# Kernel optimization log

Hardware: AMD Instinct MI355X
Metric: run time of the kernel (lower is better)

Reference implementation:

```python
import jax, jax.numpy as jnp
import numpy as np

# Module constants (from init_kwargs)
MAP_BBOX = (-5.0, -5.0, 5.0, 5.0)  # h1, w1, h2, w2
V_BBOX = (0.0, 3.0)
MAP_RES = (64, 64)
V_RES = 8
XYZ_TO_H, XYZ_TO_W, XYZ_TO_V = 0, 1, 2
SCALE = 4
PCN_H = 64


def mish(x):
    return x * jnp.tanh(jax.nn.softplus(x))


def conv_d2(x, w):
    # 3x3 conv, dilation 2, padding 2, stride 1, no bias (NCHW / OIHW)
    return jax.lax.conv_general_dilated(
        x, w, window_strides=(1, 1), padding=((2, 2), (2, 2)),
        rhs_dilation=(2, 2), dimension_numbers=('NCHW', 'OIHW', 'NCHW'))


def maxpool3s2(x):
    # MaxPool2d(kernel=3, stride=2, padding=1); torch pads with -inf
    return jax.lax.reduce_window(
        x, -jnp.inf, jax.lax.max,
        window_dimensions=(1, 1, 3, 3), window_strides=(1, 1, 2, 2),
        padding=((0, 0), (0, 0), (1, 1), (1, 1)))


def setup_inputs() -> dict:
    key = jax.random.key(0)
    k1, k2, k3, k4, k5 = jax.random.split(key, 5)
    N, H, W = 64, 256, 256
    B = 8
    return {
        'rgb': jax.random.normal(k1, (N, 3, H, W), dtype=jnp.float32),
        'surf_xyz': jax.random.normal(k2, (N, 3, H, W), dtype=jnp.float32),
        'W1': jax.random.normal(k3, (PCN_H, 3, 3, 3), dtype=jnp.float32) * 0.1,
        'W2': jax.random.normal(k4, (PCN_H, PCN_H, 3, 3), dtype=jnp.float32) * 0.05,
        'index': jax.random.randint(k5, (N,), 0, B, dtype=jnp.int32),
        'batch_size': B,
    }


def reference(rgb, surf_xyz, W1, W2, index, batch_size):
    N, _, H, W = surf_xyz.shape
    s = SCALE
    Hs, Ws = H // s, W // s

    # avg_pool2d(rgb, 4)
    surf_rgb = rgb.reshape(N, 3, Hs, s, Ws, s).mean(axis=(3, 5))
    # subsampled xyz: surf_xyz[:, :, 2::4, 2::4]
    sxyz = surf_xyz[:, :, s // 2::s, s // 2::s]  # (N,3,Hs,Ws)
    _index = jnp.broadcast_to(index[:, None, None], (N, Hs, Ws))

    # rgb_conv_net: conv -> mish -> maxpool -> conv -> mish -> maxpool (dropout=0)
    feat = maxpool3s2(mish(conv_d2(rgb, W1)))
    feat = maxpool3s2(mish(conv_d2(feat, W2)))  # (N, h, Hs, Ws)

    # flatten  (valid_points is None path)
    hdim = feat.shape[1]
    flat_features = feat.transpose(0, 2, 3, 1).reshape(-1, hdim)   # (M, h)
    flat_xyz = sxyz.transpose(0, 2, 3, 1).reshape(-1, 3)           # (M, 3)
    flat_rgb = surf_rgb.transpose(0, 2, 3, 1).reshape(-1, 3)       # (M, 3)
    flat_index = _index.reshape(-1)                                # (M,)

    # coord_to_grid (float->int cast truncates toward zero, matching torch .long())
    map_h, map_w = MAP_RES
    h1, w1, h2, w2 = MAP_BBOX
    v1, v2 = V_BBOX
    hs = ((flat_xyz[:, XYZ_TO_H] - h1) * map_h / (h2 - h1)).astype(jnp.int32)
    ws = ((flat_xyz[:, XYZ_TO_W] - w1) * map_w / (w2 - w1)).astype(jnp.int32)
    vs = ((flat_xyz[:, XYZ_TO_V] - v1) * V_RES / (v2 - v1)).astype(jnp.int32)
    valid = ((hs >= 0) & (hs < map_h) & (ws >= 0) & (ws < map_w)
             & (vs >= 0) & (vs < V_RES))

    B, V = batch_size, V_RES
    P = B * V * map_h * map_w
    lin = ((flat_index * V + vs) * map_h + hs) * map_w + ws
    # route invalid points to a dummy segment that gets dropped
    lin_safe = jnp.where(valid, lin, P)

    sums = jax.ops.segment_sum(flat_features, lin_safe, num_segments=P + 1)[:P]
    rgbs = jax.ops.segment_sum(flat_rgb, lin_safe, num_segments=P + 1)[:P]
    counts = jax.ops.segment_sum(
        jnp.ones_like(lin_safe), lin_safe, num_segments=P + 1)[:P]

    feature_map = sums.reshape(B, V, map_h, map_w, hdim).transpose(0, 4, 1, 2, 3)
    rgb_map = rgbs.reshape(B, V, map_h, map_w, 3).transpose(0, 4, 1, 2, 3)
    feature_counts = counts.reshape(B, V, map_h, map_w)[:, None]
    return feature_map, feature_counts, rgb_map
```

## Files before the change

kernel.cpp:

```cpp
#include <hip/hip_runtime.h>
#include <hip/hip_bf16.h>
#include <math.h>

#define N_IMG 64
#define CH    64
#define F1_R  136
#define F1_C  136
#define F1_IMG_STRIDE ((size_t)F1_R * F1_C * 64)
#define F1_ROW_STRIDE (F1_C * 64)
#define FEAT1_BYTES ((size_t)N_IMG * F1_IMG_STRIDE * 2)
#define LINPT_BYTES (262144 * 4)

#define OUT_CNT_BASE 16777216
#define OUT_RGB_BASE 17039360

typedef short bf16x8 __attribute__((ext_vector_type(8)));
typedef float f32x4  __attribute__((ext_vector_type(4)));

__device__ __forceinline__ float fast_mish(float x) {
    float xc = fminf(x, 20.0f);
    float t  = __expf(xc);
    float n  = t * (t + 2.0f);
    float y  = x * n / (n + 2.0f);
    return (x > 20.0f) ? x : y;
}

__device__ __forceinline__ unsigned short f2bf(float f) {
    unsigned u = __float_as_uint(f);
    unsigned r = (u + 0x7FFFu + ((u >> 16) & 1u)) >> 16;
    return (unsigned short)r;
}

__global__ __launch_bounds__(256) void w2cvt_kernel(
    const float* __restrict__ w2, unsigned short* __restrict__ w2bf)
{
    int i = blockIdx.x * 256 + threadIdx.x;
    if (i < 36864) {
        int t  = i >> 12;
        int co = (i >> 6) & 63;
        int ci = i & 63;
        w2bf[i] = f2bf(w2[(co * 64 + ci) * 9 + t]);
    }
}

__global__ __launch_bounds__(256) void point_kernel(
    const float* __restrict__ rgb,
    const float* __restrict__ sxyz,
    const int*   __restrict__ index,
    float*       __restrict__ out,
    int*         __restrict__ lin_pt)
{
    int p = blockIdx.x * 256 + threadIdx.x;
    int n  = p >> 12;
    int r  = p & 4095;
    int hs = r >> 6;
    int ws = r & 63;

    int row = hs * 4 + 2, col = ws * 4 + 2;
    const float* sx = sxyz + (size_t)n * 3 * 65536;
    float X = sx[row * 256 + col];
    float Y = sx[65536 + row * 256 + col];
    float Z = sx[2 * 65536 + row * 256 + col];

    int hb = (int)(((X + 5.0f) * 64.0f) / 10.0f);
    int wb = (int)(((Y + 5.0f) * 64.0f) / 10.0f);
    int vb = (int)((Z * 8.0f) / 3.0f);
    bool valid = (hb >= 0) & (hb < 64) & (wb >= 0) & (wb < 64) & (vb >= 0) & (vb < 8);

    int b   = index[n];
    int lin = ((b * 8 + vb) * 64 + hb) * 64 + wb;
    lin_pt[p] = valid ? lin : -1;

    if (valid) {
        atomicAdd(out + OUT_CNT_BASE + lin, 1.0f);
        int rem = lin & 32767;
        #pragma unroll
        for (int c = 0; c < 3; c++) {
            const float* rg = rgb + (size_t)(n * 3 + c) * 65536;
            float s = 0.0f;
            #pragma unroll
            for (int i = 0; i < 4; i++)
                #pragma unroll
                for (int j = 0; j < 4; j++)
                    s += rg[(hs * 4 + i) * 256 + (ws * 4 + j)];
            atomicAdd(out + OUT_RGB_BASE + b * 98304 + c * 32768 + rem, s * 0.0625f);
        }
    }
}

__global__ __launch_bounds__(1024) void conv1_mfma_kernel(
    const float* __restrict__ rgb,
    const float* __restrict__ w1,
    __hip_bfloat16* __restrict__ feat1)
{
    int b2 = ((blockIdx.x & 7) << 9) + (blockIdx.x >> 3);
    const int n  = b2 >> 6;
    const int pr = b2 & 63;
    const int tid  = threadIdx.x;
    const int lane = tid & 63;
    const int w    = tid >> 6;

    __shared__ __align__(16) char smem[81920];
    unsigned short* wlds = (unsigned short*)smem;
    unsigned short* in_t = (unsigned short*)(smem + 4096);

    for (int i = tid; i < 2048; i += 1024) {
        int co = i >> 5, k = i & 31;
        wlds[i] = (k < 27) ? f2bf(w1[co * 27 + k]) : (unsigned short)0;
    }
    {
        const float* img = rgb + (size_t)n * 3 * 65536;
        for (int i = tid; i < 7144; i += 1024) {
            unsigned short v = 0;
            if (i < 7128) {
                int ci  = i / 2376;
                int rem = i - ci * 2376;
                int rr  = rem / 264;
                int cc  = rem - rr * 264;
                int gy  = 4 * pr - 3 + rr;
                int gx  = cc - 2;
                if (gy >= 0 && gy < 256 && gx >= 0 && gx < 256)
                    v = f2bf(img[ci * 65536 + gy * 256 + gx]);
            }
            in_t[i] = v;
        }
    }
    __syncthreads();

    int boff[8];
    #pragma unroll
    for (int j = 0; j < 8; j++) {
        int k = ((lane >> 4) << 3) + j;
        if (k < 27) {
            int ci = k / 9, t = k - 9 * ci, ky = t / 3, kx = t - 3 * ky;
            boff[j] = (ci * 2376 + 2 * ky * 264 + 2 * kx + (lane & 15)) * 2;
        } else {
            boff[j] = 7128 * 2;
        }
    }

    bf16x8 a[4];
    #pragma unroll
    for (int mt = 0; mt < 4; mt++)
        a[mt] = *reinterpret_cast<const bf16x8*>(
            wlds + (mt * 16 + (lane & 15)) * 32 + ((lane >> 4) << 3));

    f32x4 acc[5][4];
    #pragma unroll
    for (int tt = 0; tt < 5; tt++)
        #pragma unroll
        for (int mt = 0; mt < 4; mt++)
            acc[tt][mt] = (f32x4){0.f, 0.f, 0.f, 0.f};

    const char* in_b = (const char*)in_t;
    #pragma unroll
    for (int tt = 0; tt < 5; tt++) {
        int t5 = w * 5 + tt;
        int r  = t5 >> 4;
        int x0 = (t5 & 15) << 4;
        int base = (r * 264 + x0) * 2;
        unsigned short e[8];
        #pragma unroll
        for (int j = 0; j < 8; j++)
            e[j] = *reinterpret_cast<const unsigned short*>(in_b + base + boff[j]);
        bf16x8 b;
        #pragma unroll
        for (int j = 0; j < 8; j++) b[j] = (short)e[j];
        #pragma unroll
        for (int mt = 0; mt < 4; mt++)
            acc[tt][mt] = __builtin_amdgcn_mfma_f32_16x16x32_bf16(a[mt], b, acc[tt][mt], 0, 0, 0);
    }

    __syncthreads();

    unsigned short* pool = (unsigned short*)smem;
    const int ybase = 4 * pr - 1;

    #pragma unroll
    for (int p = 0; p < 2; p++) {
        #pragma unroll
        for (int tt = 0; tt < 5; tt++) {
            int t5 = w * 5 + tt;
            int r  = t5 >> 4;
            int x  = ((t5 & 15) << 4) + (lane & 15);
            bool dead = (ybase + r) < 0;
            #pragma unroll
            for (int m2 = 0; m2 < 2; m2++) {
                int mt  = p * 2 + m2;
                int col = m2 * 16 + ((lane >> 4) << 2);
                unsigned long long pk = 0;
                #pragma unroll
                for (int q = 0; q < 4; q++) {
                    float v = dead ? -INFINITY : fast_mish(acc[tt][mt][q]);
                    pk |= (unsigned long long)f2bf(v) << (16 * q);
                }
                int byte = (((r * 256 + x) * 32) + col) * 2;
                byte ^= (x & 7) << 4;
                *reinterpret_cast<unsigned long long*>((char*)pool + byte) = pk;
            }
        }
        __syncthreads();
        for (int i = tid; i < 8192; i += 1024) {
            int pp = i >> 12;
            int c  = (i >> 5) & 127;
            int cl = i & 31;
            float m = -INFINITY;
            #pragma unroll
            for (int dy = 0; dy < 3; dy++) {
                int lr = 2 * pp + dy;
                #pragma unroll
                for (int dx = 0; dx < 3; dx++) {
                    int x = 2 * c - 1 + dx;
                    if (x < 0) continue;
                    int byte = ((((lr * 256) + x) * 32) + cl) * 2;
                    byte ^= (x & 7) << 4;
                    unsigned short hv = *reinterpret_cast<const unsigned short*>((char*)pool + byte);
                    m = fmaxf(m, __uint_as_float((unsigned)hv << 16));
                }
            }
            unsigned short* dst = (unsigned short*)(feat1 + (size_t)n * F1_IMG_STRIDE
                + (size_t)(2 * pr + pp + 4) * F1_ROW_STRIDE + (size_t)(c + 4) * 64 + p * 32 + cl);
            *dst = f2bf(m);
        }
        __syncthreads();
    }
}

__global__ __launch_bounds__(640, 5) void conv2_mfma_kernel(
    const __hip_bfloat16* __restrict__ feat1,
    const unsigned short* __restrict__ w2bf,
    const int*   __restrict__ lin_pt,
    float*       __restrict__ out)
{
    int b2 = ((blockIdx.x & 7) << 9) + (blockIdx.x >> 3);
    const int n   = b2 >> 6;
    const int pr  = (b2 >> 1) & 31;
    const int ch2 = b2 & 1;
    const int tid  = threadIdx.x;
    const int lane = tid & 63;
    const int w    = tid >> 6;
    const int lrow = w >> 1;
    const int chalf = w & 1;
    const int y = 4 * pr - 1 + lrow;

    __shared__ __align__(16) char smem[40960];

    for (int i = tid; i < 18432; i += 640) {
        int t    = i >> 11;
        int co32 = (i >> 6) & 31;
        int ci   = i & 63;
        int byte = (((((t << 5) + co32) << 6) + ci) << 1) ^ ((co32 & 7) << 4);
        *reinterpret_cast<unsigned short*>(smem + byte) =
            w2bf[((t << 6) + ch2 * 32 + co32) * 64 + ci];
    }
    __syncthreads();

    f32x4 acc[2][4];
    #pragma unroll
    for (int mt = 0; mt < 2; mt++)
        #pragma unroll
        for (int nt = 0; nt < 4; nt++)
            acc[mt][nt] = (f32x4){0.f, 0.f, 0.f, 0.f};

    const __hip_bfloat16* bbase = feat1 + (size_t)n * F1_IMG_STRIDE
        + ((size_t)(y + 2) * F1_C + (lane & 15) + chalf * 64 + 2) * 64
        + ((lane >> 4) << 3);

    #pragma unroll
    for (int ky = 0; ky < 3; ky++) {
        #pragma unroll
        for (int kx = 0; kx < 3; kx++) {
            const int t = ky * 3 + kx;
            #pragma unroll
            for (int s = 0; s < 2; s++) {
                bf16x8 a[2];
                #pragma unroll
                for (int mt = 0; mt < 2; mt++) {
                    int co32 = mt * 16 + (lane & 15);
                    int abyte = (((((t << 5) + co32) << 6) + (s << 5) + ((lane >> 4) << 3)) << 1)
                                ^ ((co32 & 7) << 4);
                    a[mt] = *reinterpret_cast<const bf16x8*>(smem + abyte);
                }
                const __hip_bfloat16* bp = bbase + (ky * 2 * F1_C + kx * 2) * 64 + s * 32;
                #pragma unroll
                for (int nt = 0; nt < 4; nt++) {
                    bf16x8 b = *reinterpret_cast<const bf16x8*>(bp + nt * 1024);
                    #pragma unroll
                    for (int mt = 0; mt < 2; mt++)
                        acc[mt][nt] = __builtin_amdgcn_mfma_f32_16x16x32_bf16(
                            a[mt], b, acc[mt][nt], 0, 0, 0);
                }
            }
        }
    }

    __syncthreads();

    const bool deadrow = (y < 0);
    #pragma unroll
    for (int nt = 0; nt < 4; nt++) {
        int col = chalf * 64 + nt * 16 + (lane & 15);
        #pragma unroll
        for (int mt = 0; mt < 2; mt++) {
            int cl0 = mt * 16 + ((lane >> 4) << 2);
            unsigned long long pk = 0;
            #pragma unroll
            for (int r4 = 0; r4 < 4; r4++) {
                float v = deadrow ? -INFINITY : fast_mish(acc[mt][nt][r4]);
                pk |= (unsigned long long)f2bf(v) << (16 * r4);
            }
            int byte = ((((lrow * 128 + col) * 32) + cl0) * 2) ^ ((col & 7) << 4);
            *reinterpret_cast<unsigned long long*>(smem + byte) = pk;
        }
    }
    __syncthreads();

    const int pbase = (n << 12) + ((pr << 1) << 6);
    for (int i = tid; i < 4096; i += 640) {
        int pp = i >> 11;
        int c  = (i >> 5) & 63;
        int cl = i & 31;
        float m = -INFINITY;
        #pragma unroll
        for (int dy = 0; dy < 3; dy++) {
            int lr = 2 * pp + dy;
            #pragma unroll
            for (int dx = 0; dx < 3; dx++) {
                int x = 2 * c - 1 + dx;
                if (x < 0 || x > 127) continue;
                int byte = ((((lr * 128 + x) * 32) + cl) * 2) ^ ((x & 7) << 4);
                unsigned short hv = *reinterpret_cast<const unsigned short*>(smem + byte);
                m = fmaxf(m, __uint_as_float((unsigned)hv << 16));
            }
        }
        int lin = lin_pt[pbase + (pp << 6) + c];
        if (lin >= 0)
            atomicAdd(out + (size_t)(lin >> 15) * 2097152
                          + (size_t)(ch2 * 32 + cl) * 32768 + (lin & 32767), m);
    }
}

extern "C" void kernel_launch(void* const* d_in, const int* in_sizes, int n_in,
                              void* d_out, int out_size, void* d_ws, size_t ws_size,
                              hipStream_t stream)
{
    const float* rgb   = (const float*)d_in[0];
    const float* sxyz  = (const float*)d_in[1];
    const float* w1    = (const float*)d_in[2];
    const float* w2    = (const float*)d_in[3];
    const int*   index = (const int*)d_in[4];
    float* out = (float*)d_out;

    __hip_bfloat16* feat1 = (__hip_bfloat16*)d_ws;
    int* lin_pt = (int*)((char*)d_ws + FEAT1_BYTES);
    unsigned short* w2bf = (unsigned short*)((char*)d_ws + FEAT1_BYTES + LINPT_BYTES);

    hipMemsetAsync(d_out, 0, (size_t)out_size * 4, stream);
    hipMemsetAsync(d_ws, 0, FEAT1_BYTES, stream);

    w2cvt_kernel<<<144, 256, 0, stream>>>(w2, w2bf);
    point_kernel<<<1024, 256, 0, stream>>>(rgb, sxyz, index, out, lin_pt);
    conv1_mfma_kernel<<<4096, 1024, 0, stream>>>(rgb, w1, feat1);
    conv2_mfma_kernel<<<4096, 640, 0, stream>>>(feat1, w2bf, lin_pt, out);
}
```

Before: 1.241 ms.

## Split conv2 from pooling and scatter to drop overlapping halo rows

Conv2 no longer recomputes the overlapping halo row for each pooled-row pair. Each block now computes 4 distinct rows and writes mish output as bf16 to a workspace buffer. A separate pool-and-scatter kernel then takes the 3x3 max and does the atomic adds, skipping invalid points early. The work runs in two chunks of 32 images so the intermediate stays small and may stay in cache. The cost is an extra global write and read of the pre-pool activations plus more kernel launches.

Result: slower. 1.364 ms (+9.9%).

```diff
diff --git a/kernel.cpp b/kernel.cpp
--- a/kernel.cpp
+++ b/kernel.cpp
@@ -10,6 +10,7 @@
 #define F1_ROW_STRIDE (F1_C * 64)
 #define FEAT1_BYTES ((size_t)N_IMG * F1_IMG_STRIDE * 2)
 #define LINPT_BYTES (262144 * 4)
+#define W2BF_BYTES (36864 * 2)
 
 #define OUT_CNT_BASE 16777216
 #define OUT_RGB_BASE 17039360
@@ -226,26 +227,27 @@
     }
 }
 
-__global__ __launch_bounds__(640, 5) void conv2_mfma_kernel(
+__global__ __launch_bounds__(512, 4) void conv2_mfma_kernel(
     const __hip_bfloat16* __restrict__ feat1,
     const unsigned short* __restrict__ w2bf,
-    const int*   __restrict__ lin_pt,
-    float*       __restrict__ out)
-{
-    int b2 = ((blockIdx.x & 7) << 9) + (blockIdx.x >> 3);
-    const int n   = b2 >> 6;
-    const int pr  = (b2 >> 1) & 31;
-    const int ch2 = b2 & 1;
+    __hip_bfloat16* __restrict__ pre2,
+    int n0)
+{
+    int b2 = ((blockIdx.x & 7) << 8) + (blockIdx.x >> 3);
+    const int nl  = b2 >> 6;
+    const int ch2 = (b2 >> 5) & 1;
+    const int rq  = b2 & 31;
+    const int n   = n0 + nl;
     const int tid  = threadIdx.x;
     const int lane = tid & 63;
     const int w    = tid >> 6;
     const int lrow = w >> 1;
     const int chalf = w & 1;
-    const int y = 4 * pr - 1 + lrow;
-
-    __shared__ __align__(16) char smem[40960];
-
-    for (int i = tid; i < 18432; i += 640) {
+    const int y = 4 * rq + lrow;
+
+    __shared__ __align__(16) char smem[36864];
+
+    for (int i = tid; i < 18432; i += 512) {
         int t    = i >> 11;
         int co32 = (i >> 6) & 31;
         int ci   = i & 63;
@@ -294,50 +296,66 @@
         }
     }
 
-    __syncthreads();
-
-    const bool deadrow = (y < 0);
     #pragma unroll
     for (int nt = 0; nt < 4; nt++) {
         int col = chalf * 64 + nt * 16 + (lane & 15);
         #pragma unroll
         for (int mt = 0; mt < 2; mt++) {
-            int cl0 = mt * 16 + ((lane >> 4) << 2);
+            int co4 = ch2 * 32 + mt * 16 + ((lane >> 4) << 2);
             unsigned long long pk = 0;
             #pragma unroll
-            for (int r4 = 0; r4 < 4; r4++) {
-                float v = deadrow ? -INFINITY : fast_mish(acc[mt][nt][r4]);
-                pk |= (unsigned long long)f2bf(v) << (16 * r4);
-            }
-            int byte = ((((lrow * 128 + col) * 32) + cl0) * 2) ^ ((col & 7) << 4);
-            *reinterpret_cast<unsigned long long*>(smem + byte) = pk;
-        }
-    }
-    __syncthreads();
-
-    const int pbase = (n << 12) + ((pr << 1) << 6);
-    for (int i = tid; i < 4096; i += 640) {
-        int pp = i >> 11;
-        int c  = (i >> 5) & 63;
-        int cl = i & 31;
-        float m = -INFINITY;
-        #pragma unroll
-        for (int dy = 0; dy < 3; dy++) {
-            int lr = 2 * pp + dy;
-            #pragma unroll
-            for (int dx = 0; dx < 3; dx++) {
-                int x = 2 * c - 1 + dx;
-                if (x < 0 || x > 127) continue;
-                int byte = ((((lr * 128 + x) * 32) + cl) * 2) ^ ((x & 7) << 4);
-                unsigned short hv = *reinterpret_cast<const unsigned short*>(smem + byte);
-                m = fmaxf(m, __uint_as_float((unsigned)hv << 16));
-            }
-        }
-        int lin = lin_pt[pbase + (pp << 6) + c];
-        if (lin >= 0)
-            atomicAdd(out + (size_t)(lin >> 15) * 2097152
-                          + (size_t)(ch2 * 32 + cl) * 32768 + (lin & 32767), m);
-    }
+            for (int r4 = 0; r4 < 4; r4++)
+                pk |= (unsigned long long)f2bf(fast_mish(acc[mt][nt][r4])) << (16 * r4);
+            *reinterpret_cast<unsigned long long*>(
+                pre2 + (((size_t)(nl * 128 + y) * 128 + col) * 64 + co4)) = pk;
+        }
+    }
+}
+
+__global__ __launch_bounds__(256) void pool2_scatter_kernel(
+    const __hip_bfloat16* __restrict__ pre2,
+    const int*   __restrict__ lin_pt,
+    float*       __restrict__ out,
+    int n0)
+{
+    int b2 = ((blockIdx.x & 7) << 8) + (blockIdx.x >> 3);
+    const int nl = b2 >> 6;
+    const int ph = b2 & 63;
+    const int pw  = threadIdx.x >> 2;
+    const int cog = threadIdx.x & 3;
+
+    int lin = lin_pt[((n0 + nl) << 12) + (ph << 6) + pw];
+    if (lin < 0) return;
+
+    float m[16];
+    #pragma unroll
+    for (int k = 0; k < 16; k++) m[k] = -INFINITY;
+
+    #pragma unroll
+    for (int dy = 0; dy < 3; dy++) {
+        int yy = 2 * ph - 1 + dy;
+        if (yy < 0 || yy > 127) continue;
+        #pragma unroll
+        for (int dx = 0; dx < 3; dx++) {
+            int xx = 2 * pw - 1 + dx;
+            if (xx < 0 || xx > 127) continue;
+            const unsigned short* p = (const unsigned short*)(pre2
+                + ((size_t)(nl * 128 + yy) * 128 + xx) * 64 + cog * 16);
+            #pragma unroll
+            for (int h = 0; h < 2; h++) {
+                bf16x8 v = *reinterpret_cast<const bf16x8*>(p + h * 8);
+                #pragma unroll
+                for (int j = 0; j < 8; j++)
+                    m[h * 8 + j] = fmaxf(m[h * 8 + j],
+                        __uint_as_float((unsigned)(unsigned short)v[j] << 16));
+            }
+        }
+    }
+
+    float* base = out + (size_t)(lin >> 15) * 2097152 + (lin & 32767);
+    #pragma unroll
+    for (int k = 0; k < 16; k++)
+        atomicAdd(base + (size_t)(cog * 16 + k) * 32768, m[k]);
 }
 
 extern "C" void kernel_launch(void* const* d_in, const int* in_sizes, int n_in,
@@ -354,6 +372,7 @@
     __hip_bfloat16* feat1 = (__hip_bfloat16*)d_ws;
     int* lin_pt = (int*)((char*)d_ws + FEAT1_BYTES);
     unsigned short* w2bf = (unsigned short*)((char*)d_ws + FEAT1_BYTES + LINPT_BYTES);
+    __hip_bfloat16* pre2 = (__hip_bfloat16*)((char*)d_ws + FEAT1_BYTES + LINPT_BYTES + W2BF_BYTES);
 
     hipMemsetAsync(d_out, 0, (size_t)out_size * 4, stream);
     hipMemsetAsync(d_ws, 0, FEAT1_BYTES, stream);
@@ -361,5 +380,8 @@
     w2cvt_kernel<<<144, 256, 0, stream>>>(w2, w2bf);
     point_kernel<<<1024, 256, 0, stream>>>(rgb, sxyz, index, out, lin_pt);
     conv1_mfma_kernel<<<4096, 1024, 0, stream>>>(rgb, w1, feat1);
-    conv2_mfma_kernel<<<4096, 640, 0, stream>>>(feat1, w2bf, lin_pt, out);
-}
+    for (int c = 0; c < 2; c++) {
+        conv2_mfma_kernel<<<2048, 512, 0, stream>>>(feat1, w2bf, pre2, c * 32);
+        pool2_scatter_kernel<<<2048, 256, 0, stream>>>(pre2, lin_pt, out, c * 32);
+    }
+}
```
